# Performance work log

Measured on AMD Instinct MI355X. Metric: run time of the kernel, lower is better.

## Reference

```python
import jax, jax.numpy as jnp
import numpy as np

B, H, KVH, D, HID = 32, 32, 8, 128, 4096
WIN, MAX_SEQ = 4096, 4096
START_POS = 3000
CURRENT_POS = 3000  # circular index into sliding-window cache

def nearest_32(n):
    return ((n + 31) // 32) * 32

PAD_L = min(nearest_32(START_POS + 1), WIN)  # 3008

def setup_inputs() -> dict:
    key = jax.random.key(0)
    k1, k2, k3 = jax.random.split(key, 3)
    x = jax.random.normal(k1, (1, 1, B, HID), jnp.float32) * 0.02
    wqkv = jax.random.normal(k2, (HID, (H + 2 * KVH) * D), jnp.float32) * 0.02
    wo = jax.random.normal(k3, (HID, HID), jnp.float32) * 0.02
    cache_k = jnp.zeros((B, KVH, WIN, D), jnp.float32)
    cache_v = jnp.zeros((B, KVH, WIN, D), jnp.float32)
    # RoPE tables (rotate-half convention, cos/sin of shape [max_seq_len, head_dim])
    inv_freq = 1.0 / (10000.0 ** (jnp.arange(0, D, 2, dtype=jnp.float32) / D))
    t = jnp.arange(MAX_SEQ, dtype=jnp.float32)
    freqs = jnp.outer(t, inv_freq)                      # [S, D/2]
    emb = jnp.concatenate([freqs, freqs], axis=-1)      # [S, D]
    cos_cached = jnp.cos(emb)
    sin_cached = jnp.sin(emb)
    # additive mask: 0 for valid cache positions (<= start_pos), -1e9 for tile padding
    pos = jnp.arange(PAD_L)
    row = jnp.where(pos <= START_POS, 0.0, -1e9).astype(jnp.float32)
    attn_mask = jnp.broadcast_to(row, (1, H, B, PAD_L))
    return {"x": x, "wqkv": wqkv, "wo": wo, "cache_k": cache_k, "cache_v": cache_v,
            "cos_cached": cos_cached, "sin_cached": sin_cached, "attn_mask": attn_mask,
            "start_pos": START_POS, "current_pos": CURRENT_POS}

def _rotate_half(u):
    return jnp.concatenate([-u[..., D // 2:], u[..., :D // 2]], axis=-1)

def reference(x, wqkv, wo, cache_k, cache_v, cos_cached, sin_cached, attn_mask,
              start_pos, current_pos):
    # fused QKV projection: x is (1,1,B,HID) decode token
    xqkv = x[0, 0] @ wqkv                               # [B, (H+2KVH)*D]
    q = xqkv[:, :H * D].reshape(B, H, D)
    k = xqkv[:, H * D:(H + KVH) * D].reshape(B, KVH, D)
    v = xqkv[:, (H + KVH) * D:].reshape(B, KVH, D)
    # RoPE at position start_pos
    cos = cos_cached[start_pos]                         # [D]
    sin = sin_cached[start_pos]
    q = q * cos + _rotate_half(q) * sin
    k = k * cos + _rotate_half(k) * sin
    # sliding-window circular KV-cache update at current_pos
    cache_k = cache_k.at[:, :, current_pos, :].set(k)
    cache_v = cache_v.at[:, :, current_pos, :].set(v)
    keys = cache_k[:, :, :PAD_L, :]                     # [B, KVH, L, D]
    vals = cache_v[:, :, :PAD_L, :]
    # grouped-query attention
    G = H // KVH
    qg = q.reshape(B, KVH, G, D)
    scores = jnp.einsum('bkgd,bkld->bkgl', qg, keys) / jnp.sqrt(jnp.float32(D))
    mask = jnp.transpose(attn_mask[0], (1, 0, 2)).reshape(B, KVH, G, PAD_L)
    probs = jax.nn.softmax(scores + mask, axis=-1)
    ctx = jnp.einsum('bkgl,bkld->bkgd', probs, vals).reshape(B, H * D)
    dense = ctx @ wo                                    # [B, HID]
    return dense.reshape(1, 1, B, HID)
```

## Files before the change

### kernel.cpp

```cpp
#include <hip/hip_runtime.h>
#include <hip/hip_bf16.h>

#define B 32
#define H 32
#define KVH 8
#define D 128
#define HID 4096
#define NQKV 6144
#define WIN 4096
#define PADL_MAX 3008
#define KS1 32
#define KS4 32

#define OFF_P1   0
#define OFF_QR   (OFF_P1 + KS1*B*NQKV)
#define OFF_KR   (OFF_QR + B*H*D)
#define OFF_VV   (OFF_KR + B*KVH*D)
#define OFF_CTX  (OFF_VV + B*KVH*D)
#define OFF_P4   (OFF_CTX + B*H*D)

typedef float vf4 __attribute__((ext_vector_type(4)));
typedef float vf2 __attribute__((ext_vector_type(2)));

__device__ __forceinline__ vf4 nt4(const float* p) {
  return __builtin_nontemporal_load((const vf4*)p);
}
__device__ __forceinline__ vf2 nt2(const float* p) {
  return __builtin_nontemporal_load((const vf2*)p);
}

__global__ __launch_bounds__(256) void k_qkv(const float* __restrict__ x,
                                             const float* __restrict__ wqkv,
                                             float* __restrict__ P1) {
  const int ks = blockIdx.y;
  const int col = blockIdx.x * 512 + threadIdx.x * 2;
  const int k0 = ks * 128;
  float2 acc[32];
#pragma unroll
  for (int b = 0; b < 32; ++b) acc[b] = make_float2(0.f, 0.f);
  const float* wp = wqkv + (size_t)k0 * NQKV + col;
  for (int kk = 0; kk < 128; ++kk) {
    const vf2 w2 = nt2(wp + (size_t)kk * NQKV);
    const int xi = k0 + kk;
#pragma unroll
    for (int b = 0; b < 32; ++b) {
      const float xv = x[b * HID + xi];
      acc[b].x = fmaf(xv, w2[0], acc[b].x);
      acc[b].y = fmaf(xv, w2[1], acc[b].y);
    }
  }
  float* op = P1 + (size_t)ks * (B * NQKV) + col;
#pragma unroll
  for (int b = 0; b < 32; ++b) *(float2*)(op + (size_t)b * NQKV) = acc[b];
}

__global__ __launch_bounds__(256) void k_rope_reduce(const float* __restrict__ P1,
                                                     const float* __restrict__ cosc,
                                                     const float* __restrict__ sinc,
                                                     const int* __restrict__ spp,
                                                     float* __restrict__ qr,
                                                     float* __restrict__ kr,
                                                     float* __restrict__ vv) {
  const int t = blockIdx.x * 256 + threadIdx.x;
  const int sp = *spp;
  if (t < B * (H + KVH) * 64) {
    const int b = t / ((H + KVH) * 64);
    const int r = t % ((H + KVH) * 64);
    const int h = r >> 6;
    const int d = r & 63;
    const int base = b * NQKV + h * D + d;
    float sA = 0.f, sB = 0.f;
#pragma unroll
    for (int s = 0; s < KS1; ++s) {
      sA += P1[(size_t)s * (B * NQKV) + base];
      sB += P1[(size_t)s * (B * NQKV) + base + 64];
    }
    const float cA = cosc[sp * D + d],      snA = sinc[sp * D + d];
    const float cB = cosc[sp * D + d + 64], snB = sinc[sp * D + d + 64];
    const float oA = sA * cA - sB * snA;
    const float oB = sB * cB + sA * snB;
    if (h < H) {
      qr[b * (H * D) + h * D + d] = oA;
      qr[b * (H * D) + h * D + d + 64] = oB;
    } else {
      const int kvh = h - H;
      kr[b * (KVH * D) + kvh * D + d] = oA;
      kr[b * (KVH * D) + kvh * D + d + 64] = oB;
    }
  } else {
    const int i = t - B * (H + KVH) * 64;
    const int b = i >> 10, c = i & 1023;
    float s = 0.f;
#pragma unroll
    for (int ss = 0; ss < KS1; ++ss)
      s += P1[(size_t)ss * (B * NQKV) + b * NQKV + (H + KVH) * D + c];
    vv[i] = s;
  }
}

__global__ __launch_bounds__(1024) void k_attn(const float* __restrict__ cache_k,
                                               const float* __restrict__ cache_v,
                                               const float* __restrict__ qr,
                                               const float* __restrict__ kr,
                                               const float* __restrict__ vv,
                                               const int* __restrict__ spp,
                                               const int* __restrict__ cpp,
                                               float* __restrict__ ctx) {
  __shared__ float sl[4 * PADL_MAX];
  __shared__ float sq[4 * D];
  __shared__ float red[16];
  __shared__ float mg[4], inv[4];
  const int b = blockIdx.x >> 3, kv = blockIdx.x & 7;
  const int sp = *spp, cp = *cpp;
  const int L = sp;
  const int tid = threadIdx.x;
  const int wave = tid >> 6, lane = tid & 63;
  const size_t kvbase = (size_t)(b * KVH + kv) * WIN * D;
  const float scale = 0.08838834764831845f;

  if (tid < 512) sq[tid] = qr[b * (H * D) + kv * 4 * D + tid] * scale;
  __syncthreads();

  const int grp = tid >> 3;
  const int c = tid & 7;
  vf4 ql[4][4];
#pragma unroll
  for (int g = 0; g < 4; ++g)
#pragma unroll
    for (int t = 0; t < 4; ++t)
      ql[g][t] = *(const vf4*)(sq + g * D + (t * 8 + c) * 4);

  const float* krow = kr + (b * KVH + kv) * D;
#pragma unroll 2
  for (int l0 = 0; l0 < 3072; l0 += 128) {
    const int l = l0 + grp;
    const float* kp = (l == cp) ? krow : (cache_k + kvbase + (size_t)l * D);
    float s0 = 0.f, s1 = 0.f, s2 = 0.f, s3 = 0.f;
#pragma unroll
    for (int t = 0; t < 4; ++t) {
      const vf4 k4 = nt4(kp + (t * 8 + c) * 4);
      s0 += ql[0][t][0] * k4[0] + ql[0][t][1] * k4[1] + ql[0][t][2] * k4[2] + ql[0][t][3] * k4[3];
      s1 += ql[1][t][0] * k4[0] + ql[1][t][1] * k4[1] + ql[1][t][2] * k4[2] + ql[1][t][3] * k4[3];
      s2 += ql[2][t][0] * k4[0] + ql[2][t][1] * k4[1] + ql[2][t][2] * k4[2] + ql[2][t][3] * k4[3];
      s3 += ql[3][t][0] * k4[0] + ql[3][t][1] * k4[1] + ql[3][t][2] * k4[2] + ql[3][t][3] * k4[3];
    }
#pragma unroll
    for (int m = 1; m <= 4; m <<= 1) {
      s0 += __shfl_xor(s0, m);
      s1 += __shfl_xor(s1, m);
      s2 += __shfl_xor(s2, m);
      s3 += __shfl_xor(s3, m);
    }
    if (c == 0 && l <= L) {
      sl[0 * PADL_MAX + l] = s0;
      sl[1 * PADL_MAX + l] = s1;
      sl[2 * PADL_MAX + l] = s2;
      sl[3 * PADL_MAX + l] = s3;
    }
  }
  __syncthreads();

  {
    const int g = tid >> 8, i = tid & 255, w4 = (tid >> 6) & 3;
    float m = -1e30f;
    for (int l = i; l <= L; l += 256) m = fmaxf(m, sl[g * PADL_MAX + l]);
#pragma unroll
    for (int mm = 1; mm <= 32; mm <<= 1) m = fmaxf(m, __shfl_xor(m, mm));
    if (lane == 0) red[g * 4 + w4] = m;
    __syncthreads();
    if (i == 0)
      mg[g] = fmaxf(fmaxf(red[g * 4], red[g * 4 + 1]),
                    fmaxf(red[g * 4 + 2], red[g * 4 + 3]));
    __syncthreads();
    const float mgv = mg[g];
    float psum = 0.f;
    for (int l = i; l <= L; l += 256) {
      const float e = __expf(sl[g * PADL_MAX + l] - mgv);
      sl[g * PADL_MAX + l] = e;
      psum += e;
    }
#pragma unroll
    for (int mm = 1; mm <= 32; mm <<= 1) psum += __shfl_xor(psum, mm);
    if (lane == 0) red[g * 4 + w4] = psum;
    __syncthreads();
    if (i == 0)
      inv[g] = 1.f / (red[g * 4] + red[g * 4 + 1] + red[g * 4 + 2] + red[g * 4 + 3]);
    __syncthreads();
  }

  const int half = lane >> 5, j = lane & 31;
  float o[4][4];
#pragma unroll
  for (int g = 0; g < 4; ++g)
#pragma unroll
    for (int cc = 0; cc < 4; ++cc) o[g][cc] = 0.f;
  const float* vrow = vv + (b * KVH + kv) * D;
#pragma unroll 2
  for (int p = wave; p < 1504; p += 16) {
    const int l = 2 * p + half;
    const float* vp = (l == cp) ? vrow : (cache_v + kvbase + (size_t)l * D);
    const vf4 v4 = nt4(vp + 4 * j);
#pragma unroll
    for (int g = 0; g < 4; ++g) {
      const float e = (l <= L) ? sl[g * PADL_MAX + l] : 0.f;
      o[g][0] = fmaf(e, v4[0], o[g][0]);
      o[g][1] = fmaf(e, v4[1], o[g][1]);
      o[g][2] = fmaf(e, v4[2], o[g][2]);
      o[g][3] = fmaf(e, v4[3], o[g][3]);
    }
  }
#pragma unroll
  for (int g = 0; g < 4; ++g)
#pragma unroll
    for (int cc = 0; cc < 4; ++cc) o[g][cc] += __shfl_xor(o[g][cc], 32);

  __syncthreads();
  if (lane < 32) {
#pragma unroll
    for (int g = 0; g < 4; ++g)
      *(float4*)&sl[wave * 512 + g * 128 + 4 * j] =
          make_float4(o[g][0], o[g][1], o[g][2], o[g][3]);
  }
  __syncthreads();
  if (tid < 512) {
    const int g = tid >> 7, d = tid & 127;
    float a = 0.f;
#pragma unroll
    for (int w = 0; w < 16; ++w) a += sl[w * 512 + g * 128 + d];
    a *= inv[g];
    ctx[b * (H * D) + (kv * 4 + g) * D + d] = a;
  }
}

__global__ __launch_bounds__(256) void k_out(const float* __restrict__ ctx,
                                             const float* __restrict__ wo,
                                             float* __restrict__ P4) {
  const int ks = blockIdx.y;
  const int col = blockIdx.x * 512 + threadIdx.x * 2;
  const int k0 = ks * 128;
  float2 acc[32];
#pragma unroll
  for (int b = 0; b < 32; ++b) acc[b] = make_float2(0.f, 0.f);
  const float* wp = wo + (size_t)k0 * HID + col;
  for (int kk = 0; kk < 128; ++kk) {
    const vf2 w2 = nt2(wp + (size_t)kk * HID);
    const int xi = k0 + kk;
#pragma unroll
    for (int b = 0; b < 32; ++b) {
      const float xv = ctx[b * HID + xi];
      acc[b].x = fmaf(xv, w2[0], acc[b].x);
      acc[b].y = fmaf(xv, w2[1], acc[b].y);
    }
  }
  float* op = P4 + (size_t)ks * (B * HID) + col;
#pragma unroll
  for (int b = 0; b < 32; ++b) *(float2*)(op + (size_t)b * HID) = acc[b];
}

__global__ __launch_bounds__(256) void k_final(const float* __restrict__ P4,
                                               float* __restrict__ out) {
  const int e = (blockIdx.x * 256 + threadIdx.x) * 4;
  float4 s = make_float4(0.f, 0.f, 0.f, 0.f);
#pragma unroll
  for (int ss = 0; ss < KS4; ++ss) {
    const float4 p = *(const float4*)(P4 + (size_t)ss * (B * HID) + e);
    s.x += p.x; s.y += p.y; s.z += p.z; s.w += p.w;
  }
  *(float4*)(out + e) = s;
}

extern "C" void kernel_launch(void* const* d_in, const int* in_sizes, int n_in,
                              void* d_out, int out_size, void* d_ws, size_t ws_size,
                              hipStream_t stream) {
  const float* x       = (const float*)d_in[0];
  const float* wqkv    = (const float*)d_in[1];
  const float* wo      = (const float*)d_in[2];
  const float* cache_k = (const float*)d_in[3];
  const float* cache_v = (const float*)d_in[4];
  const float* cosc    = (const float*)d_in[5];
  const float* sinc    = (const float*)d_in[6];
  const int* spp       = (const int*)d_in[8];
  const int* cpp       = (const int*)d_in[9];
  float* ws = (float*)d_ws;

  k_qkv<<<dim3(12, 32), 256, 0, stream>>>(x, wqkv, ws + OFF_P1);
  k_rope_reduce<<<448, 256, 0, stream>>>(ws + OFF_P1, cosc, sinc, spp,
                                         ws + OFF_QR, ws + OFF_KR, ws + OFF_VV);
  k_attn<<<256, 1024, 0, stream>>>(cache_k, cache_v, ws + OFF_QR, ws + OFF_KR,
                                   ws + OFF_VV, spp, cpp, ws + OFF_CTX);
  k_out<<<dim3(8, 32), 256, 0, stream>>>(ws + OFF_CTX, wo, ws + OFF_P4);
  k_final<<<128, 256, 0, stream>>>(ws + OFF_P4, (float*)d_out);
}
```

Before: 1.131 ms.

## Split attention over sequence chunks with a separate softmax merge kernel

Splits each (batch, kv-head) attention over 8 sequence chunks processed by separate 256-thread blocks. Each block writes a partial max, sum and unnormalized output, and a new kernel combines them with log-sum-exp rescaling. This raises block count and occupancy for the bandwidth-bound KV cache scan, in exchange for an extra launch and a small global round-trip of partials.

```diff
diff --git a/kernel.cpp b/kernel.cpp
--- a/kernel.cpp
+++ b/kernel.cpp
@@ -8,9 +8,10 @@
 #define HID 4096
 #define NQKV 6144
 #define WIN 4096
-#define PADL_MAX 3008
 #define KS1 32
 #define KS4 32
+#define SCH 8
+#define CHL 384
 
 #define OFF_P1   0
 #define OFF_QR   (OFF_P1 + KS1*B*NQKV)
@@ -18,6 +19,9 @@
 #define OFF_VV   (OFF_KR + B*KVH*D)
 #define OFF_CTX  (OFF_VV + B*KVH*D)
 #define OFF_P4   (OFF_CTX + B*H*D)
+#define OFF_PM   (OFF_P4 + KS4*B*HID)
+#define OFF_PS   (OFF_PM + 8192)
+#define OFF_PO   (OFF_PS + 8192)
 
 typedef float vf4 __attribute__((ext_vector_type(4)));
 typedef float vf2 __attribute__((ext_vector_type(2)));
@@ -98,27 +102,31 @@
   }
 }
 
-__global__ __launch_bounds__(1024) void k_attn(const float* __restrict__ cache_k,
-                                               const float* __restrict__ cache_v,
-                                               const float* __restrict__ qr,
-                                               const float* __restrict__ kr,
-                                               const float* __restrict__ vv,
-                                               const int* __restrict__ spp,
-                                               const int* __restrict__ cpp,
-                                               float* __restrict__ ctx) {
-  __shared__ float sl[4 * PADL_MAX];
+__global__ __launch_bounds__(256, 4) void k_attn(const float* __restrict__ cache_k,
+                                                 const float* __restrict__ cache_v,
+                                                 const float* __restrict__ qr,
+                                                 const float* __restrict__ kr,
+                                                 const float* __restrict__ vv,
+                                                 const int* __restrict__ spp,
+                                                 const int* __restrict__ cpp,
+                                                 float* __restrict__ pM,
+                                                 float* __restrict__ pS,
+                                                 float* __restrict__ pO) {
+  __shared__ float sl[4096];
   __shared__ float sq[4 * D];
-  __shared__ float red[16];
-  __shared__ float mg[4], inv[4];
-  const int b = blockIdx.x >> 3, kv = blockIdx.x & 7;
+  const int blk = blockIdx.x;
+  const int bk = blk >> 3, chunk = blk & 7;
+  const int b = bk >> 3, kv = bk & 7;
   const int sp = *spp, cp = *cpp;
   const int L = sp;
+  const int l0 = chunk * CHL;
   const int tid = threadIdx.x;
-  const int wave = tid >> 6, lane = tid & 63;
+  const int lane = tid & 63;
   const size_t kvbase = (size_t)(b * KVH + kv) * WIN * D;
   const float scale = 0.08838834764831845f;
 
-  if (tid < 512) sq[tid] = qr[b * (H * D) + kv * 4 * D + tid] * scale;
+  sq[tid] = qr[b * (H * D) + kv * 4 * D + tid] * scale;
+  sq[tid + 256] = qr[b * (H * D) + kv * 4 * D + tid + 256] * scale;
   __syncthreads();
 
   const int grp = tid >> 3;
@@ -132,8 +140,9 @@
 
   const float* krow = kr + (b * KVH + kv) * D;
 #pragma unroll 2
-  for (int l0 = 0; l0 < 3072; l0 += 128) {
-    const int l = l0 + grp;
+  for (int pass = 0; pass < 12; ++pass) {
+    const int li = pass * 32 + grp;
+    const int l = l0 + li;
     const float* kp = (l == cp) ? krow : (cache_k + kvbase + (size_t)l * D);
     float s0 = 0.f, s1 = 0.f, s2 = 0.f, s3 = 0.f;
 #pragma unroll
@@ -151,85 +160,107 @@
       s2 += __shfl_xor(s2, m);
       s3 += __shfl_xor(s3, m);
     }
-    if (c == 0 && l <= L) {
-      sl[0 * PADL_MAX + l] = s0;
-      sl[1 * PADL_MAX + l] = s1;
-      sl[2 * PADL_MAX + l] = s2;
-      sl[3 * PADL_MAX + l] = s3;
+    if (c == 0) {
+      sl[0 * CHL + li] = s0;
+      sl[1 * CHL + li] = s1;
+      sl[2 * CHL + li] = s2;
+      sl[3 * CHL + li] = s3;
     }
   }
   __syncthreads();
 
   {
-    const int g = tid >> 8, i = tid & 255, w4 = (tid >> 6) & 3;
+    const int g = tid >> 6;
+    float sv[6];
     float m = -1e30f;
-    for (int l = i; l <= L; l += 256) m = fmaxf(m, sl[g * PADL_MAX + l]);
+#pragma unroll
+    for (int k = 0; k < 6; ++k) {
+      const int li = k * 64 + lane;
+      const bool valid = (l0 + li) <= L;
+      sv[k] = valid ? sl[g * CHL + li] : -1e30f;
+      m = fmaxf(m, sv[k]);
+    }
 #pragma unroll
     for (int mm = 1; mm <= 32; mm <<= 1) m = fmaxf(m, __shfl_xor(m, mm));
-    if (lane == 0) red[g * 4 + w4] = m;
-    __syncthreads();
-    if (i == 0)
-      mg[g] = fmaxf(fmaxf(red[g * 4], red[g * 4 + 1]),
-                    fmaxf(red[g * 4 + 2], red[g * 4 + 3]));
-    __syncthreads();
-    const float mgv = mg[g];
     float psum = 0.f;
-    for (int l = i; l <= L; l += 256) {
-      const float e = __expf(sl[g * PADL_MAX + l] - mgv);
-      sl[g * PADL_MAX + l] = e;
+#pragma unroll
+    for (int k = 0; k < 6; ++k) {
+      const int li = k * 64 + lane;
+      const float e = (sv[k] > -1e29f) ? __expf(sv[k] - m) : 0.f;
+      sl[g * CHL + li] = e;
       psum += e;
     }
 #pragma unroll
     for (int mm = 1; mm <= 32; mm <<= 1) psum += __shfl_xor(psum, mm);
-    if (lane == 0) red[g * 4 + w4] = psum;
-    __syncthreads();
-    if (i == 0)
-      inv[g] = 1.f / (red[g * 4] + red[g * 4 + 1] + red[g * 4 + 2] + red[g * 4 + 3]);
-    __syncthreads();
-  }
-
-  const int half = lane >> 5, j = lane & 31;
+    if (lane == 0) {
+      pM[blk * 4 + g] = m;
+      pS[blk * 4 + g] = psum;
+    }
+  }
+  __syncthreads();
+
+  const int hw = tid >> 5, j = tid & 31;
   float o[4][4];
 #pragma unroll
   for (int g = 0; g < 4; ++g)
 #pragma unroll
     for (int cc = 0; cc < 4; ++cc) o[g][cc] = 0.f;
   const float* vrow = vv + (b * KVH + kv) * D;
-#pragma unroll 2
-  for (int p = wave; p < 1504; p += 16) {
-    const int l = 2 * p + half;
+#pragma unroll 4
+  for (int pass = 0; pass < 48; ++pass) {
+    const int li = pass * 8 + hw;
+    const int l = l0 + li;
     const float* vp = (l == cp) ? vrow : (cache_v + kvbase + (size_t)l * D);
     const vf4 v4 = nt4(vp + 4 * j);
 #pragma unroll
     for (int g = 0; g < 4; ++g) {
-      const float e = (l <= L) ? sl[g * PADL_MAX + l] : 0.f;
+      const float e = sl[g * CHL + li];
       o[g][0] = fmaf(e, v4[0], o[g][0]);
       o[g][1] = fmaf(e, v4[1], o[g][1]);
       o[g][2] = fmaf(e, v4[2], o[g][2]);
       o[g][3] = fmaf(e, v4[3], o[g][3]);
     }
   }
+  __syncthreads();
 #pragma unroll
   for (int g = 0; g < 4; ++g)
-#pragma unroll
-    for (int cc = 0; cc < 4; ++cc) o[g][cc] += __shfl_xor(o[g][cc], 32);
-
-  __syncthreads();
-  if (lane < 32) {
-#pragma unroll
-    for (int g = 0; g < 4; ++g)
-      *(float4*)&sl[wave * 512 + g * 128 + 4 * j] =
-          make_float4(o[g][0], o[g][1], o[g][2], o[g][3]);
-  }
-  __syncthreads();
-  if (tid < 512) {
-    const int g = tid >> 7, d = tid & 127;
+    *(float4*)&sl[hw * 512 + g * 128 + 4 * j] =
+        make_float4(o[g][0], o[g][1], o[g][2], o[g][3]);
+  __syncthreads();
+#pragma unroll
+  for (int t = 0; t < 2; ++t) {
+    const int e = tid + t * 256;
+    const int g = e >> 7, d = e & 127;
     float a = 0.f;
 #pragma unroll
-    for (int w = 0; w < 16; ++w) a += sl[w * 512 + g * 128 + d];
-    a *= inv[g];
-    ctx[b * (H * D) + (kv * 4 + g) * D + d] = a;
-  }
+    for (int w = 0; w < 8; ++w) a += sl[w * 512 + g * 128 + d];
+    pO[((size_t)blk * 4 + g) * 128 + d] = a;
+  }
+}
+
+__global__ __launch_bounds__(512) void k_attn2(const float* __restrict__ pM,
+                                               const float* __restrict__ pS,
+                                               const float* __restrict__ pO,
+                                               float* __restrict__ ctx) {
+  const int bk = blockIdx.x;
+  const int b = bk >> 3, kv = bk & 7;
+  const int tid = threadIdx.x;
+  const int g = tid >> 7, d = tid & 127;
+  float m[SCH];
+  float M = -1e30f;
+#pragma unroll
+  for (int c = 0; c < SCH; ++c) {
+    m[c] = pM[(bk * SCH + c) * 4 + g];
+    M = fmaxf(M, m[c]);
+  }
+  float denom = 0.f, val = 0.f;
+#pragma unroll
+  for (int c = 0; c < SCH; ++c) {
+    const float w = __expf(m[c] - M);
+    denom = fmaf(pS[(bk * SCH + c) * 4 + g], w, denom);
+    val = fmaf(pO[((size_t)(bk * SCH + c) * 4 + g) * 128 + d], w, val);
+  }
+  ctx[b * (H * D) + (kv * 4 + g) * D + d] = val / denom;
 }
 
 __global__ __launch_bounds__(256) void k_out(const float* __restrict__ ctx,
@@ -286,8 +317,11 @@
   k_qkv<<<dim3(12, 32), 256, 0, stream>>>(x, wqkv, ws + OFF_P1);
   k_rope_reduce<<<448, 256, 0, stream>>>(ws + OFF_P1, cosc, sinc, spp,
                                          ws + OFF_QR, ws + OFF_KR, ws + OFF_VV);
-  k_attn<<<256, 1024, 0, stream>>>(cache_k, cache_v, ws + OFF_QR, ws + OFF_KR,
-                                   ws + OFF_VV, spp, cpp, ws + OFF_CTX);
+  k_attn<<<2048, 256, 0, stream>>>(cache_k, cache_v, ws + OFF_QR, ws + OFF_KR,
+                                   ws + OFF_VV, spp, cpp,
+                                   ws + OFF_PM, ws + OFF_PS, ws + OFF_PO);
+  k_attn2<<<256, 512, 0, stream>>>(ws + OFF_PM, ws + OFF_PS, ws + OFF_PO,
+                                   ws + OFF_CTX);
   k_out<<<dim3(8, 32), 256, 0, stream>>>(ws + OFF_CTX, wo, ws + OFF_P4);
   k_final<<<128, 256, 0, stream>>>(ws + OFF_P4, (float*)d_out);
 }
```

New measurement: 1.126 ms. No clear change (-0.5%).
